# Kernel tuning notes

Measured on AMD Instinct MI355X. Metric: run time of the kernel, lower is better.

## Reference

```python
import jax, jax.numpy as jnp
import numpy as np

B = 4096      # batch
F = 26        # sparse fields
V = 100000    # vocab per field
D = 64        # emb_dim
A = 64        # att_vector
ND = 13       # dense features
FEA = ND + D  # 77, BN / DNN input width
HID = [FEA, 256, 128, 64]
EPS = 1e-5


def setup_inputs() -> dict:
    key = jax.random.key(0)
    ks = jax.random.split(key, 20)
    s = 0.05  # matches .normal_(0, 0.05) init
    inp = {
        "sx": jax.random.randint(ks[0], (B, F), 0, V),
        "dx": jax.random.normal(ks[1], (B, ND), dtype=jnp.float32),
        "emb_table": jax.random.normal(ks[2], (F, V, D), dtype=jnp.float32) * s,
        "att_w_W": jax.random.normal(ks[3], (D, A), dtype=jnp.float32) * s,
        "att_w_b": jnp.zeros((A,), jnp.float32),
        "att_d_W": jax.random.normal(ks[4], (A, 1), dtype=jnp.float32) * s,
        "att_d_b": jnp.zeros((1,), jnp.float32),
        "bn_gamma": jnp.ones((FEA,), jnp.float32),
        "bn_beta": jnp.zeros((FEA,), jnp.float32),
        "w1": jax.random.normal(ks[5], (HID[0], HID[1]), dtype=jnp.float32) * s,
        "b1": jnp.zeros((HID[1],), jnp.float32),
        "w2": jax.random.normal(ks[6], (HID[1], HID[2]), dtype=jnp.float32) * s,
        "b2": jnp.zeros((HID[2],), jnp.float32),
        "w3": jax.random.normal(ks[7], (HID[2], HID[3]), dtype=jnp.float32) * s,
        "b3": jnp.zeros((HID[3],), jnp.float32),
        "wf": jax.random.normal(ks[8], (HID[3], 1), dtype=jnp.float32) * s,
        "bf": jnp.zeros((1,), jnp.float32),
    }
    return inp


def _afm_forward(sx, dx, emb_table, att_w_W, att_w_b, att_d_W, att_d_b,
                 bn_gamma, bn_beta, w1, b1, w2, b2, w3, b3, wf, bf):
    # embedding gather: [B, F, D]
    embeds = emb_table[jnp.arange(F)[None, :], sx]
    # all pairwise field interactions (upper-triangular pairs)
    i1, i2 = np.triu_indices(F, k=1)          # P = F*(F-1)/2 = 325
    bi = embeds[:, i1, :] * embeds[:, i2, :]  # [B, P, D]
    # attention MLP + softmax-weighted sum pooling over pairs
    a = jax.nn.relu(jnp.einsum("bpd,da->bpa", bi, att_w_W) + att_w_b)
    scores = jnp.einsum("bpa,ao->bpo", a, att_d_W) + att_d_b  # [B, P, 1]
    w = jax.nn.softmax(scores, axis=1)
    att_out = jnp.sum(w * bi, axis=1)         # [B, D]
    # concat with dense, batchnorm (training-mode batch stats, biased var)
    x = jnp.concatenate([att_out, dx], axis=-1)  # [B, FEA]
    mu = jnp.mean(x, axis=0)
    var = jnp.mean((x - mu) ** 2, axis=0)
    x = (x - mu) * jax.lax.rsqrt(var + EPS) * bn_gamma + bn_beta
    # DNN tower (dropout=0.0 -> identity) + final linear + sigmoid
    x = jax.nn.relu(x @ w1 + b1)
    x = jax.nn.relu(x @ w2 + b2)
    x = jax.nn.relu(x @ w3 + b3)
    out = jax.nn.sigmoid(x @ wf + bf)
    return jnp.squeeze(out, axis=-1)          # [B]


def reference(sx, dx, emb_table, att_w_W, att_w_b, att_d_W, att_d_b,
              bn_gamma, bn_beta, w1, b1, w2, b2, w3, b3, wf, bf):
    return _afm_forward(sx, dx, emb_table, att_w_W, att_w_b, att_d_W, att_d_b,
                        bn_gamma, bn_beta, w1, b1, w2, b2, w3, b3, wf, bf)
```

## Files before the change

kernel.cpp:

```cpp
#include <hip/hip_runtime.h>
#include <hip/hip_bf16.h>
#include <math.h>

#define BSZ   4096
#define F     26
#define VOC   100000
#define D     64
#define AD    64
#define ND    13
#define FEA   77
#define NPAIR 325
#define NPAD  336
#define MT    21
#define EP    68
#define SCP   384
#define H1    256
#define H2    128
#define H3    64
#define EPSF  1e-5f
#define MROW  8

typedef __attribute__((ext_vector_type(8))) short short8;
typedef __attribute__((ext_vector_type(4))) float f32x4;

union FragU { short8 s; unsigned int u[4]; };

__device__ __forceinline__ unsigned int pk2bf(float a, float b) {
  __hip_bfloat162 h = __float22bfloat162_rn(make_float2(a, b));
  return *reinterpret_cast<unsigned int*>(&h);
}
__device__ __forceinline__ unsigned short f2bf(float f) {
  unsigned int u = __float_as_uint(f);
  u += 0x7fffu + ((u >> 16) & 1u);
  return (unsigned short)(u >> 16);
}
template<int CTRL>
__device__ __forceinline__ float dpp_add(float x) {
  int xi = __builtin_bit_cast(int, x);
  int yi = __builtin_amdgcn_update_dpp(xi, xi, CTRL, 0xf, 0xf, false);
  return x + __builtin_bit_cast(float, yi);
}
__device__ __forceinline__ float row16_sum(float x) {
  x = dpp_add<0xB1>(x);
  x = dpp_add<0x4E>(x);
  x = dpp_add<0x124>(x);
  x = dpp_add<0x128>(x);
  return x;
}

__global__ __launch_bounds__(256, 4) void k_attn(
    const int* __restrict__ sx, const float* __restrict__ dx,
    const float* __restrict__ emb, const float* __restrict__ attW,
    const float* __restrict__ attb, const float* __restrict__ attdW,
    const float* __restrict__ attdb, float* __restrict__ x)
{
  __shared__ __align__(16) float e_all[4][27 * EP];
  __shared__ __align__(16) float sc_all[4][SCP];
  __shared__ unsigned short pt[NPAD];

  const int t    = threadIdx.x;
  const int lane = t & 63;
  const int wv   = t >> 6;
  const int b    = blockIdx.x * 4 + wv;

  for (int p = t; p < NPAD; p += 256) {
    int f1 = 26, f2 = 26;
    if (p < NPAIR) {
      int i = 0, rem = p;
      while (rem >= F - 1 - i) { rem -= F - 1 - i; ++i; }
      f1 = i; f2 = i + 1 + rem;
    }
    pt[p] = (unsigned short)(f1 | (f2 << 8));
  }

  float* e_w  = e_all[wv];
  float* sc_w = sc_all[wv];

  {
    int rowsv[7]; float4 vv[7];
    #pragma unroll
    for (int i = 0; i < 7; ++i) {
      int k = lane + 64 * i, f = k >> 4;
      rowsv[i] = (f < F) ? sx[b * F + f] : 0;
    }
    #pragma unroll
    for (int i = 0; i < 7; ++i) {
      int k = lane + 64 * i, f = k >> 4, q = k & 15;
      float4 v = {0.f, 0.f, 0.f, 0.f};
      if (f < F) v = *(const float4*)&emb[((size_t)f * VOC + rowsv[i]) * D + q * 4];
      vv[i] = v;
    }
    #pragma unroll
    for (int i = 0; i < 7; ++i) {
      int k = lane + 64 * i, f = k >> 4, q = k & 15;
      if (f < 27) *(float4*)&e_w[f * EP + q * 4] = vv[i];
    }
  }

  short8 bfrag[2][4];
  float bj[4], dwj[4];
  {
    const int kb = (lane >> 4) * 8;
    const int cl = lane & 15;
    #pragma unroll
    for (int kk = 0; kk < 2; ++kk)
      #pragma unroll
      for (int n = 0; n < 4; ++n)
        #pragma unroll
        for (int j = 0; j < 8; ++j) {
          int k = kk * 32 + kb + j;
          bfrag[kk][n][j] = (short)f2bf(attW[k * AD + n * 16 + cl]);
        }
    #pragma unroll
    for (int n = 0; n < 4; ++n) {
      bj[n]  = attb[n * 16 + cl];
      dwj[n] = attdW[n * 16 + cl];
    }
  }
  const float db0 = attdb[0];

  __syncthreads();

  const int row16 = lane & 15;
  const int kgrp  = lane >> 4;
  for (int m = 0; m < MT; ++m) {
    const int row = m * 16 + row16;
    const unsigned short pp = pt[row];
    const float* r1 = &e_w[(pp & 0xff) * EP];
    const float* r2 = &e_w[(pp >> 8) * EP];
    FragU a0, a1;
    {
      const int k0 = kgrp * 8;
      float4 x0 = *(const float4*)&r1[k0];
      float4 x1 = *(const float4*)&r1[k0 + 4];
      float4 y0 = *(const float4*)&r2[k0];
      float4 y1 = *(const float4*)&r2[k0 + 4];
      a0.u[0] = pk2bf(x0.x * y0.x, x0.y * y0.y);
      a0.u[1] = pk2bf(x0.z * y0.z, x0.w * y0.w);
      a0.u[2] = pk2bf(x1.x * y1.x, x1.y * y1.y);
      a0.u[3] = pk2bf(x1.z * y1.z, x1.w * y1.w);
      float4 x2 = *(const float4*)&r1[32 + k0];
      float4 x3 = *(const float4*)&r1[32 + k0 + 4];
      float4 y2 = *(const float4*)&r2[32 + k0];
      float4 y3 = *(const float4*)&r2[32 + k0 + 4];
      a1.u[0] = pk2bf(x2.x * y2.x, x2.y * y2.y);
      a1.u[1] = pk2bf(x2.z * y2.z, x2.w * y2.w);
      a1.u[2] = pk2bf(x3.x * y3.x, x3.y * y3.y);
      a1.u[3] = pk2bf(x3.z * y3.z, x3.w * y3.w);
    }
    f32x4 acc[4];
    #pragma unroll
    for (int n = 0; n < 4; ++n) {
      f32x4 z = {0.f, 0.f, 0.f, 0.f};
      acc[n] = __builtin_amdgcn_mfma_f32_16x16x32_bf16(a0.s, bfrag[0][n], z, 0, 0, 0);
      acc[n] = __builtin_amdgcn_mfma_f32_16x16x32_bf16(a1.s, bfrag[1][n], acc[n], 0, 0, 0);
    }
    float v4[4];
    #pragma unroll
    for (int r = 0; r < 4; ++r) {
      float val = 0.f;
      #pragma unroll
      for (int n = 0; n < 4; ++n)
        val += fmaxf(acc[n][r] + bj[n], 0.f) * dwj[n];
      v4[r] = row16_sum(val) + db0;
    }
    if (row16 == 0) {
      float4 o = {v4[0], v4[1], v4[2], v4[3]};
      *(float4*)&sc_w[m * 16 + kgrp * 4] = o;
    }
  }

  float sv[6], ev[6];
  float mx = -1e30f;
  #pragma unroll
  for (int i = 0; i < 6; ++i) {
    int idx = lane + 64 * i;
    sv[i] = (idx < NPAIR) ? sc_w[idx] : -1e30f;
    mx = fmaxf(mx, sv[i]);
  }
  #pragma unroll
  for (int off = 32; off; off >>= 1) mx = fmaxf(mx, __shfl_xor(mx, off));
  float s = 0.f;
  #pragma unroll
  for (int i = 0; i < 6; ++i) {
    int idx = lane + 64 * i;
    ev[i] = (idx < NPAIR) ? __expf(sv[i] - mx) : 0.f;
    s += ev[i];
  }
  #pragma unroll
  for (int off = 32; off; off >>= 1) s += __shfl_xor(s, off);
  const float invZ = 1.f / s;
  #pragma unroll
  for (int i = 0; i < 6; ++i) {
    int idx = lane + 64 * i;
    if (idx < NPAD) sc_w[idx] = ev[i] * invZ;
  }

  const int dblk = lane >> 3;
  const int g    = lane & 7;
  float acc[8] = {0,0,0,0,0,0,0,0};
  for (int it = 0; it < NPAD / 8; ++it) {
    const int p = g + 8 * it;
    const float wgt = sc_w[p];
    const unsigned short pp = pt[p];
    const float* r1 = &e_w[(pp & 0xff) * EP + dblk * 8];
    const float* r2 = &e_w[(pp >> 8) * EP + dblk * 8];
    float4 x0 = *(const float4*)r1;
    float4 x1 = *(const float4*)(r1 + 4);
    float4 y0 = *(const float4*)r2;
    float4 y1 = *(const float4*)(r2 + 4);
    acc[0] = fmaf(wgt, x0.x * y0.x, acc[0]);
    acc[1] = fmaf(wgt, x0.y * y0.y, acc[1]);
    acc[2] = fmaf(wgt, x0.z * y0.z, acc[2]);
    acc[3] = fmaf(wgt, x0.w * y0.w, acc[3]);
    acc[4] = fmaf(wgt, x1.x * y1.x, acc[4]);
    acc[5] = fmaf(wgt, x1.y * y1.y, acc[5]);
    acc[6] = fmaf(wgt, x1.z * y1.z, acc[6]);
    acc[7] = fmaf(wgt, x1.w * y1.w, acc[7]);
  }
  #pragma unroll
  for (int j = 0; j < 8; ++j) {
    acc[j] = dpp_add<0xB1>(acc[j]);
    acc[j] = dpp_add<0x4E>(acc[j]);
    acc[j] = dpp_add<0x124>(acc[j]);
  }
  if (g == 0) {
    float* xo = &x[(size_t)b * FEA + dblk * 8];
    #pragma unroll
    for (int j = 0; j < 8; ++j) xo[j] = acc[j];
  }
  if (lane >= 8 && lane < 8 + ND) {
    x[(size_t)b * FEA + D + (lane - 8)] = dx[b * ND + (lane - 8)];
  }
}

__global__ __launch_bounds__(256) void k_bnstats(
    const float* __restrict__ x, const float* __restrict__ gamma,
    const float* __restrict__ beta, float* __restrict__ scale,
    float* __restrict__ shift)
{
  const int f = blockIdx.x;
  const int t = threadIdx.x;
  const int lane = t & 63;
  const int wv = t >> 6;
  double s = 0.0, s2 = 0.0;
  for (int b = t; b < BSZ; b += 256) {
    float v = x[(size_t)b * FEA + f];
    s += v;
    s2 += (double)v * v;
  }
  #pragma unroll
  for (int off = 32; off; off >>= 1) {
    s += __shfl_xor(s, off);
    s2 += __shfl_xor(s2, off);
  }
  __shared__ double rs[4], rs2[4];
  if (lane == 0) { rs[wv] = s; rs2[wv] = s2; }
  __syncthreads();
  if (t == 0) {
    double S = 0.0, S2 = 0.0;
    #pragma unroll
    for (int i = 0; i < 4; ++i) { S += rs[i]; S2 += rs2[i]; }
    double mu = S / BSZ;
    double var = S2 / BSZ - mu * mu;
    float g = gamma[f];
    float scl = (float)((double)g / sqrt(var + (double)EPSF));
    scale[f] = scl;
    shift[f] = beta[f] - (float)mu * scl;
  }
}

__global__ __launch_bounds__(256) void k_mlp(
    const float* __restrict__ x,
    const float* __restrict__ scale, const float* __restrict__ shift,
    const float* __restrict__ w1, const float* __restrict__ b1,
    const float* __restrict__ w2, const float* __restrict__ b2,
    const float* __restrict__ w3, const float* __restrict__ b3,
    const float* __restrict__ wf, const float* __restrict__ bf,
    float* __restrict__ out)
{
  __shared__ float xn[MROW][80];
  __shared__ float h1s[MROW][H1];
  __shared__ float h2s[MROW][H2];
  __shared__ float h3s[MROW][H3];
  const int t = threadIdx.x;
  const int b0 = blockIdx.x * MROW;

  for (int k = t; k < MROW * FEA; k += 256) {
    int r = k / FEA, f = k % FEA;
    xn[r][f] = x[(size_t)(b0 + r) * FEA + f] * scale[f] + shift[f];
  }
  __syncthreads();

  {
    float acc[MROW];
    const float bb = b1[t];
    #pragma unroll
    for (int r = 0; r < MROW; ++r) acc[r] = bb;
    for (int d = 0; d < FEA; ++d) {
      float wv = w1[d * H1 + t];
      #pragma unroll
      for (int r = 0; r < MROW; ++r) acc[r] = fmaf(xn[r][d], wv, acc[r]);
    }
    #pragma unroll
    for (int r = 0; r < MROW; ++r) h1s[r][t] = fmaxf(acc[r], 0.f);
  }
  __syncthreads();

  {
    const int j = t & 127;
    const int rb = (t >> 7) * 4;
    float acc[4];
    const float bb = b2[j];
    #pragma unroll
    for (int r = 0; r < 4; ++r) acc[r] = bb;
    for (int k = 0; k < H1; ++k) {
      float wv = w2[k * H2 + j];
      #pragma unroll
      for (int r = 0; r < 4; ++r) acc[r] = fmaf(h1s[rb + r][k], wv, acc[r]);
    }
    #pragma unroll
    for (int r = 0; r < 4; ++r) h2s[rb + r][j] = fmaxf(acc[r], 0.f);
  }
  __syncthreads();

  {
    const int j = t & 63;
    const int rb = (t >> 6) * 2;
    float acc[2];
    const float bb = b3[j];
    #pragma unroll
    for (int r = 0; r < 2; ++r) acc[r] = bb;
    for (int k = 0; k < H2; ++k) {
      float wv = w3[k * H3 + j];
      #pragma unroll
      for (int r = 0; r < 2; ++r) acc[r] = fmaf(h2s[rb + r][k], wv, acc[r]);
    }
    #pragma unroll
    for (int r = 0; r < 2; ++r) h3s[rb + r][j] = fmaxf(acc[r], 0.f);
  }
  __syncthreads();

  if (t < MROW) {
    float acc = bf[0];
    for (int k = 0; k < H3; ++k) acc = fmaf(h3s[t][k], wf[k], acc);
    out[b0 + t] = 1.f / (1.f + __expf(-acc));
  }
}

extern "C" void kernel_launch(void* const* d_in, const int* in_sizes, int n_in,
                              void* d_out, int out_size, void* d_ws, size_t ws_size,
                              hipStream_t stream) {
  const int*   sx    = (const int*)  d_in[0];
  const float* dx    = (const float*)d_in[1];
  const float* emb   = (const float*)d_in[2];
  const float* attW  = (const float*)d_in[3];
  const float* attb  = (const float*)d_in[4];
  const float* attdW = (const float*)d_in[5];
  const float* attdb = (const float*)d_in[6];
  const float* gamma = (const float*)d_in[7];
  const float* beta  = (const float*)d_in[8];
  const float* w1    = (const float*)d_in[9];
  const float* b1    = (const float*)d_in[10];
  const float* w2    = (const float*)d_in[11];
  const float* b2    = (const float*)d_in[12];
  const float* w3    = (const float*)d_in[13];
  const float* b3    = (const float*)d_in[14];
  const float* wf    = (const float*)d_in[15];
  const float* bf    = (const float*)d_in[16];
  float* out = (float*)d_out;

  float* x     = (float*)d_ws;
  float* scale = x + (size_t)BSZ * FEA;
  float* shift = scale + FEA;

  k_attn<<<BSZ / 4, 256, 0, stream>>>(sx, dx, emb, attW, attb, attdW, attdb, x);
  k_bnstats<<<FEA, 256, 0, stream>>>(x, gamma, beta, scale, shift);
  k_mlp<<<BSZ / MROW, 256, 0, stream>>>(x, scale, shift, w1, b1, w2, b2, w3, b3,
                                        wf, bf, out);
}
```

Baseline: 72.55 us.

## Fuse attention scoring, online softmax and weighted pooling into one pass

Replaces the three-phase attention (score pairs into shared memory, softmax, then a second pass recomputing pairwise products for the weighted sum) with a single flash-style online-softmax loop. The fp32 pairwise products already built for the MFMA A fragments are reused and accumulated with running-max rescaling, so the shared score buffer and the second LDS sweep over embedding rows go away. In exchange it adds per-tile shuffles for the max and score broadcast, conditional rescaling, and 16 extra accumulator registers per lane, which may raise register pressure under the 4-block launch bound.

```diff
diff --git a/kernel.cpp b/kernel.cpp
--- a/kernel.cpp
+++ b/kernel.cpp
@@ -13,7 +13,6 @@
 #define NPAD  336
 #define MT    21
 #define EP    68
-#define SCP   384
 #define H1    256
 #define H2    128
 #define H3    64
@@ -55,7 +54,6 @@
     const float* __restrict__ attdb, float* __restrict__ x)
 {
   __shared__ __align__(16) float e_all[4][27 * EP];
-  __shared__ __align__(16) float sc_all[4][SCP];
   __shared__ unsigned short pt[NPAD];
 
   const int t    = threadIdx.x;
@@ -73,8 +71,7 @@
     pt[p] = (unsigned short)(f1 | (f2 << 8));
   }
 
-  float* e_w  = e_all[wv];
-  float* sc_w = sc_all[wv];
+  float* e_w = e_all[wv];
 
   {
     int rowsv[7]; float4 vv[7];
@@ -121,33 +118,39 @@
 
   __syncthreads();
 
-  const int row16 = lane & 15;
-  const int kgrp  = lane >> 4;
+  const int row16  = lane & 15;
+  const int kgrp   = lane >> 4;
+  const int kgrp4  = kgrp * 4;
+  const int k0     = kgrp * 8;
+  const int selsrc = ((row16 >> 2) << 4) | row16;
+
+  float pacc_a[8] = {0,0,0,0,0,0,0,0};
+  float pacc_b[8] = {0,0,0,0,0,0,0,0};
+  float m_run = -3.0e38f, l_lane = 0.f;
+
   for (int m = 0; m < MT; ++m) {
-    const int row = m * 16 + row16;
-    const unsigned short pp = pt[row];
+    const int prow = m * 16 + row16;
+    const unsigned short pp = pt[prow];
     const float* r1 = &e_w[(pp & 0xff) * EP];
     const float* r2 = &e_w[(pp >> 8) * EP];
+    float4 x0 = *(const float4*)&r1[k0];
+    float4 x1 = *(const float4*)&r1[k0 + 4];
+    float4 y0 = *(const float4*)&r2[k0];
+    float4 y1 = *(const float4*)&r2[k0 + 4];
+    float4 x2 = *(const float4*)&r1[32 + k0];
+    float4 x3 = *(const float4*)&r1[32 + k0 + 4];
+    float4 y2 = *(const float4*)&r2[32 + k0];
+    float4 y3 = *(const float4*)&r2[32 + k0 + 4];
+    float ba[8] = {x0.x*y0.x, x0.y*y0.y, x0.z*y0.z, x0.w*y0.w,
+                   x1.x*y1.x, x1.y*y1.y, x1.z*y1.z, x1.w*y1.w};
+    float bb[8] = {x2.x*y2.x, x2.y*y2.y, x2.z*y2.z, x2.w*y2.w,
+                   x3.x*y3.x, x3.y*y3.y, x3.z*y3.z, x3.w*y3.w};
     FragU a0, a1;
-    {
-      const int k0 = kgrp * 8;
-      float4 x0 = *(const float4*)&r1[k0];
-      float4 x1 = *(const float4*)&r1[k0 + 4];
-      float4 y0 = *(const float4*)&r2[k0];
-      float4 y1 = *(const float4*)&r2[k0 + 4];
-      a0.u[0] = pk2bf(x0.x * y0.x, x0.y * y0.y);
-      a0.u[1] = pk2bf(x0.z * y0.z, x0.w * y0.w);
-      a0.u[2] = pk2bf(x1.x * y1.x, x1.y * y1.y);
-      a0.u[3] = pk2bf(x1.z * y1.z, x1.w * y1.w);
-      float4 x2 = *(const float4*)&r1[32 + k0];
-      float4 x3 = *(const float4*)&r1[32 + k0 + 4];
-      float4 y2 = *(const float4*)&r2[32 + k0];
-      float4 y3 = *(const float4*)&r2[32 + k0 + 4];
-      a1.u[0] = pk2bf(x2.x * y2.x, x2.y * y2.y);
-      a1.u[1] = pk2bf(x2.z * y2.z, x2.w * y2.w);
-      a1.u[2] = pk2bf(x3.x * y3.x, x3.y * y3.y);
-      a1.u[3] = pk2bf(x3.z * y3.z, x3.w * y3.w);
-    }
+    a0.u[0] = pk2bf(ba[0], ba[1]); a0.u[1] = pk2bf(ba[2], ba[3]);
+    a0.u[2] = pk2bf(ba[4], ba[5]); a0.u[3] = pk2bf(ba[6], ba[7]);
+    a1.u[0] = pk2bf(bb[0], bb[1]); a1.u[1] = pk2bf(bb[2], bb[3]);
+    a1.u[2] = pk2bf(bb[4], bb[5]); a1.u[3] = pk2bf(bb[6], bb[7]);
+
     f32x4 acc[4];
     #pragma unroll
     for (int n = 0; n < 4; ++n) {
@@ -164,70 +167,49 @@
         val += fmaxf(acc[n][r] + bj[n], 0.f) * dwj[n];
       v4[r] = row16_sum(val) + db0;
     }
-    if (row16 == 0) {
-      float4 o = {v4[0], v4[1], v4[2], v4[3]};
-      *(float4*)&sc_w[m * 16 + kgrp * 4] = o;
-    }
-  }
-
-  float sv[6], ev[6];
-  float mx = -1e30f;
-  #pragma unroll
-  for (int i = 0; i < 6; ++i) {
-    int idx = lane + 64 * i;
-    sv[i] = (idx < NPAIR) ? sc_w[idx] : -1e30f;
-    mx = fmaxf(mx, sv[i]);
-  }
-  #pragma unroll
-  for (int off = 32; off; off >>= 1) mx = fmaxf(mx, __shfl_xor(mx, off));
-  float s = 0.f;
-  #pragma unroll
-  for (int i = 0; i < 6; ++i) {
-    int idx = lane + 64 * i;
-    ev[i] = (idx < NPAIR) ? __expf(sv[i] - mx) : 0.f;
-    s += ev[i];
-  }
-  #pragma unroll
-  for (int off = 32; off; off >>= 1) s += __shfl_xor(s, off);
-  const float invZ = 1.f / s;
-  #pragma unroll
-  for (int i = 0; i < 6; ++i) {
-    int idx = lane + 64 * i;
-    if (idx < NPAD) sc_w[idx] = ev[i] * invZ;
-  }
-
-  const int dblk = lane >> 3;
-  const int g    = lane & 7;
-  float acc[8] = {0,0,0,0,0,0,0,0};
-  for (int it = 0; it < NPAD / 8; ++it) {
-    const int p = g + 8 * it;
-    const float wgt = sc_w[p];
-    const unsigned short pp = pt[p];
-    const float* r1 = &e_w[(pp & 0xff) * EP + dblk * 8];
-    const float* r2 = &e_w[(pp >> 8) * EP + dblk * 8];
-    float4 x0 = *(const float4*)r1;
-    float4 x1 = *(const float4*)(r1 + 4);
-    float4 y0 = *(const float4*)r2;
-    float4 y1 = *(const float4*)(r2 + 4);
-    acc[0] = fmaf(wgt, x0.x * y0.x, acc[0]);
-    acc[1] = fmaf(wgt, x0.y * y0.y, acc[1]);
-    acc[2] = fmaf(wgt, x0.z * y0.z, acc[2]);
-    acc[3] = fmaf(wgt, x0.w * y0.w, acc[3]);
-    acc[4] = fmaf(wgt, x1.x * y1.x, acc[4]);
-    acc[5] = fmaf(wgt, x1.y * y1.y, acc[5]);
-    acc[6] = fmaf(wgt, x1.z * y1.z, acc[6]);
-    acc[7] = fmaf(wgt, x1.w * y1.w, acc[7]);
-  }
+    float sel = v4[0];
+    sel = ((row16 & 3) == 1) ? v4[1] : sel;
+    sel = ((row16 & 3) == 2) ? v4[2] : sel;
+    sel = ((row16 & 3) == 3) ? v4[3] : sel;
+    const float s_p = __shfl(sel, selsrc);
+    float lm = -3.0e38f;
+    #pragma unroll
+    for (int r = 0; r < 4; ++r) {
+      int p = m * 16 + kgrp4 + r;
+      if (p < NPAIR) lm = fmaxf(lm, v4[r]);
+    }
+    lm = fmaxf(lm, __shfl_xor(lm, 16));
+    lm = fmaxf(lm, __shfl_xor(lm, 32));
+    if (lm > m_run) {
+      const float scl = __expf(m_run - lm);
+      l_lane *= scl;
+      #pragma unroll
+      for (int j = 0; j < 8; ++j) { pacc_a[j] *= scl; pacc_b[j] *= scl; }
+      m_run = lm;
+    }
+    const float w = (prow < NPAIR) ? __expf(s_p - m_run) : 0.f;
+    l_lane += w;
+    #pragma unroll
+    for (int j = 0; j < 8; ++j) {
+      pacc_a[j] = fmaf(w, ba[j], pacc_a[j]);
+      pacc_b[j] = fmaf(w, bb[j], pacc_b[j]);
+    }
+  }
+
+  const float l_tot = row16_sum(l_lane);
+  const float invZ = 1.f / l_tot;
   #pragma unroll
   for (int j = 0; j < 8; ++j) {
-    acc[j] = dpp_add<0xB1>(acc[j]);
-    acc[j] = dpp_add<0x4E>(acc[j]);
-    acc[j] = dpp_add<0x124>(acc[j]);
-  }
-  if (g == 0) {
-    float* xo = &x[(size_t)b * FEA + dblk * 8];
-    #pragma unroll
-    for (int j = 0; j < 8; ++j) xo[j] = acc[j];
+    pacc_a[j] = row16_sum(pacc_a[j]);
+    pacc_b[j] = row16_sum(pacc_b[j]);
+  }
+  if (row16 == 0) {
+    float* xo = &x[(size_t)b * FEA + kgrp * 8];
+    #pragma unroll
+    for (int j = 0; j < 8; ++j) xo[j] = pacc_a[j] * invZ;
+    float* xo2 = &x[(size_t)b * FEA + 32 + kgrp * 8];
+    #pragma unroll
+    for (int j = 0; j < 8; ++j) xo2[j] = pacc_b[j] * invZ;
   }
   if (lane >= 8 && lane < 8 + ND) {
     x[(size_t)b * FEA + D + (lane - 8)] = dx[b * ND + (lane - 8)];
```

Result: slower. 74.46 us (+2.6%).

## Store gathered embeddings as bf16 in LDS and halve MLP rows per block

Applied to the files above, without the earlier changes.

The attention kernel now packs gathered embedding rows into bf16 in shared memory with a smaller row stride, so LDS traffic for pair products and pooling is halved and occupancy may rise. Products are formed from the bf16-unpacked values, which loses precision in the weighted-sum pooling that was previously fp32. Separately, the MLP kernel processes 4 rows per block instead of 8, doubling grid size for more parallelism, and adds unroll pragmas.

```diff
diff --git a/kernel.cpp b/kernel.cpp
--- a/kernel.cpp
+++ b/kernel.cpp
@@ -12,13 +12,12 @@
 #define NPAIR 325
 #define NPAD  336
 #define MT    21
-#define EP    68
-#define SCP   384
+#define ERS   36
 #define H1    256
 #define H2    128
 #define H3    64
 #define EPSF  1e-5f
-#define MROW  8
+#define MROW  4
 
 typedef __attribute__((ext_vector_type(8))) short short8;
 typedef __attribute__((ext_vector_type(4))) float f32x4;
@@ -33,6 +32,12 @@
   unsigned int u = __float_as_uint(f);
   u += 0x7fffu + ((u >> 16) & 1u);
   return (unsigned short)(u >> 16);
+}
+__device__ __forceinline__ float bflo(unsigned int u) {
+  return __uint_as_float(u << 16);
+}
+__device__ __forceinline__ float bfhi(unsigned int u) {
+  return __uint_as_float(u & 0xffff0000u);
 }
 template<int CTRL>
 __device__ __forceinline__ float dpp_add(float x) {
@@ -54,8 +59,8 @@
     const float* __restrict__ attb, const float* __restrict__ attdW,
     const float* __restrict__ attdb, float* __restrict__ x)
 {
-  __shared__ __align__(16) float e_all[4][27 * EP];
-  __shared__ __align__(16) float sc_all[4][SCP];
+  __shared__ __align__(16) unsigned int e_all[4][27 * ERS];
+  __shared__ __align__(16) float sc_all[4][NPAD];
   __shared__ unsigned short pt[NPAD];
 
   const int t    = threadIdx.x;
@@ -73,7 +78,7 @@
     pt[p] = (unsigned short)(f1 | (f2 << 8));
   }
 
-  float* e_w  = e_all[wv];
+  unsigned int* e_w = e_all[wv];
   float* sc_w = sc_all[wv];
 
   {
@@ -93,7 +98,10 @@
     #pragma unroll
     for (int i = 0; i < 7; ++i) {
       int k = lane + 64 * i, f = k >> 4, q = k & 15;
-      if (f < 27) *(float4*)&e_w[f * EP + q * 4] = vv[i];
+      if (f < 27) {
+        uint2 o = { pk2bf(vv[i].x, vv[i].y), pk2bf(vv[i].z, vv[i].w) };
+        *(uint2*)&e_w[f * ERS + 2 * q] = o;
+      }
     }
   }
 
@@ -123,31 +131,26 @@
 
   const int row16 = lane & 15;
   const int kgrp  = lane >> 4;
+  const int ku    = kgrp * 4;
   for (int m = 0; m < MT; ++m) {
-    const int row = m * 16 + row16;
-    const unsigned short pp = pt[row];
-    const float* r1 = &e_w[(pp & 0xff) * EP];
-    const float* r2 = &e_w[(pp >> 8) * EP];
+    const int prow = m * 16 + row16;
+    const unsigned short pp = pt[prow];
+    const unsigned int* r1 = &e_w[(pp & 0xff) * ERS];
+    const unsigned int* r2 = &e_w[(pp >> 8) * ERS];
+    uint4 u1a = *(const uint4*)&r1[ku];
+    uint4 u2a = *(const uint4*)&r2[ku];
+    uint4 u1b = *(const uint4*)&r1[16 + ku];
+    uint4 u2b = *(const uint4*)&r2[16 + ku];
     FragU a0, a1;
-    {
-      const int k0 = kgrp * 8;
-      float4 x0 = *(const float4*)&r1[k0];
-      float4 x1 = *(const float4*)&r1[k0 + 4];
-      float4 y0 = *(const float4*)&r2[k0];
-      float4 y1 = *(const float4*)&r2[k0 + 4];
-      a0.u[0] = pk2bf(x0.x * y0.x, x0.y * y0.y);
-      a0.u[1] = pk2bf(x0.z * y0.z, x0.w * y0.w);
-      a0.u[2] = pk2bf(x1.x * y1.x, x1.y * y1.y);
-      a0.u[3] = pk2bf(x1.z * y1.z, x1.w * y1.w);
-      float4 x2 = *(const float4*)&r1[32 + k0];
-      float4 x3 = *(const float4*)&r1[32 + k0 + 4];
-      float4 y2 = *(const float4*)&r2[32 + k0];
-      float4 y3 = *(const float4*)&r2[32 + k0 + 4];
-      a1.u[0] = pk2bf(x2.x * y2.x, x2.y * y2.y);
-      a1.u[1] = pk2bf(x2.z * y2.z, x2.w * y2.w);
-      a1.u[2] = pk2bf(x3.x * y3.x, x3.y * y3.y);
-      a1.u[3] = pk2bf(x3.z * y3.z, x3.w * y3.w);
-    }
+    a0.u[0] = pk2bf(bflo(u1a.x)*bflo(u2a.x), bfhi(u1a.x)*bfhi(u2a.x));
+    a0.u[1] = pk2bf(bflo(u1a.y)*bflo(u2a.y), bfhi(u1a.y)*bfhi(u2a.y));
+    a0.u[2] = pk2bf(bflo(u1a.z)*bflo(u2a.z), bfhi(u1a.z)*bfhi(u2a.z));
+    a0.u[3] = pk2bf(bflo(u1a.w)*bflo(u2a.w), bfhi(u1a.w)*bfhi(u2a.w));
+    a1.u[0] = pk2bf(bflo(u1b.x)*bflo(u2b.x), bfhi(u1b.x)*bfhi(u2b.x));
+    a1.u[1] = pk2bf(bflo(u1b.y)*bflo(u2b.y), bfhi(u1b.y)*bfhi(u2b.y));
+    a1.u[2] = pk2bf(bflo(u1b.z)*bflo(u2b.z), bfhi(u1b.z)*bfhi(u2b.z));
+    a1.u[3] = pk2bf(bflo(u1b.w)*bflo(u2b.w), bfhi(u1b.w)*bfhi(u2b.w));
+
     f32x4 acc[4];
     #pragma unroll
     for (int n = 0; n < 4; ++n) {
@@ -203,20 +206,16 @@
     const int p = g + 8 * it;
     const float wgt = sc_w[p];
     const unsigned short pp = pt[p];
-    const float* r1 = &e_w[(pp & 0xff) * EP + dblk * 8];
-    const float* r2 = &e_w[(pp >> 8) * EP + dblk * 8];
-    float4 x0 = *(const float4*)r1;
-    float4 x1 = *(const float4*)(r1 + 4);
-    float4 y0 = *(const float4*)r2;
-    float4 y1 = *(const float4*)(r2 + 4);
-    acc[0] = fmaf(wgt, x0.x * y0.x, acc[0]);
-    acc[1] = fmaf(wgt, x0.y * y0.y, acc[1]);
-    acc[2] = fmaf(wgt, x0.z * y0.z, acc[2]);
-    acc[3] = fmaf(wgt, x0.w * y0.w, acc[3]);
-    acc[4] = fmaf(wgt, x1.x * y1.x, acc[4]);
-    acc[5] = fmaf(wgt, x1.y * y1.y, acc[5]);
-    acc[6] = fmaf(wgt, x1.z * y1.z, acc[6]);
-    acc[7] = fmaf(wgt, x1.w * y1.w, acc[7]);
+    uint4 w1v = *(const uint4*)&e_w[(pp & 0xff) * ERS + dblk * 4];
+    uint4 w2v = *(const uint4*)&e_w[(pp >> 8) * ERS + dblk * 4];
+    acc[0] = fmaf(wgt, bflo(w1v.x) * bflo(w2v.x), acc[0]);
+    acc[1] = fmaf(wgt, bfhi(w1v.x) * bfhi(w2v.x), acc[1]);
+    acc[2] = fmaf(wgt, bflo(w1v.y) * bflo(w2v.y), acc[2]);
+    acc[3] = fmaf(wgt, bfhi(w1v.y) * bfhi(w2v.y), acc[3]);
+    acc[4] = fmaf(wgt, bflo(w1v.z) * bflo(w2v.z), acc[4]);
+    acc[5] = fmaf(wgt, bfhi(w1v.z) * bfhi(w2v.z), acc[5]);
+    acc[6] = fmaf(wgt, bflo(w1v.w) * bflo(w2v.w), acc[6]);
+    acc[7] = fmaf(wgt, bfhi(w1v.w) * bfhi(w2v.w), acc[7]);
   }
   #pragma unroll
   for (int j = 0; j < 8; ++j) {
@@ -297,6 +296,7 @@
     const float bb = b1[t];
     #pragma unroll
     for (int r = 0; r < MROW; ++r) acc[r] = bb;
+    #pragma unroll 8
     for (int d = 0; d < FEA; ++d) {
       float wv = w1[d * H1 + t];
       #pragma unroll
@@ -309,40 +309,35 @@
 
   {
     const int j = t & 127;
-    const int rb = (t >> 7) * 4;
-    float acc[4];
+    const int rb = (t >> 7) * 2;
+    float acc[2];
     const float bb = b2[j];
-    #pragma unroll
-    for (int r = 0; r < 4; ++r) acc[r] = bb;
+    acc[0] = bb; acc[1] = bb;
+    #pragma unroll 8
     for (int k = 0; k < H1; ++k) {
       float wv = w2[k * H2 + j];
-      #pragma unroll
-      for (int r = 0; r < 4; ++r) acc[r] = fmaf(h1s[rb + r][k], wv, acc[r]);
-    }
-    #pragma unroll
-    for (int r = 0; r < 4; ++r) h2s[rb + r][j] = fmaxf(acc[r], 0.f);
+      acc[0] = fmaf(h1s[rb + 0][k], wv, acc[0]);
+      acc[1] = fmaf(h1s[rb + 1][k], wv, acc[1]);
+    }
+    h2s[rb + 0][j] = fmaxf(acc[0], 0.f);
+    h2s[rb + 1][j] = fmaxf(acc[1], 0.f);
   }
   __syncthreads();
 
   {
     const int j = t & 63;
-    const int rb = (t >> 6) * 2;
-    float acc[2];
-    const float bb = b3[j];
-    #pragma unroll
-    for (int r = 0; r < 2; ++r) acc[r] = bb;
-    for (int k = 0; k < H2; ++k) {
-      float wv = w3[k * H3 + j];
-      #pragma unroll
-      for (int r = 0; r < 2; ++r) acc[r] = fmaf(h2s[rb + r][k], wv, acc[r]);
-    }
-    #pragma unroll
-    for (int r = 0; r < 2; ++r) h3s[rb + r][j] = fmaxf(acc[r], 0.f);
+    const int r = t >> 6;
+    float acc = b3[j];
+    #pragma unroll 8
+    for (int k = 0; k < H2; ++k)
+      acc = fmaf(h2s[r][k], w3[k * H3 + j], acc);
+    h3s[r][j] = fmaxf(acc, 0.f);
   }
   __syncthreads();
 
   if (t < MROW) {
     float acc = bf[0];
+    #pragma unroll 8
     for (int k = 0; k < H3; ++k) acc = fmaf(h3s[t][k], wf[k], acc);
     out[b0 + t] = 1.f / (1.f + __expf(-acc));
   }
```

Measured after the change: 79.87 us. 1.1x slower.

## Fuse BN statistics into attention kernel and pool pairs in registers

Applied to the files above, without the earlier changes.

Removes the separate BN-stats kernel. The attention kernel now accumulates per-feature sum and sum-of-squares through atomics into 8 bucketed partial arrays, and the MLP kernel finalizes the scale and shift itself. Each lane keeps its embedding column in registers, so the weighted pair pooling becomes a fully unrolled 325-step loop using readlane broadcasts of the softmax weights instead of shared-memory loads. This saves a launch and a pass over x, at the cost of a memset, atomic contention, fp32 (rather than double) variance with the E[x^2]-mu^2 form, and much higher register pressure from the unrolled loop.

```diff
diff --git a/kernel.cpp b/kernel.cpp
--- a/kernel.cpp
+++ b/kernel.cpp
@@ -13,7 +13,6 @@
 #define NPAD  336
 #define MT    21
 #define EP    68
-#define SCP   384
 #define H1    256
 #define H2    128
 #define H3    64
@@ -47,21 +46,27 @@
   x = dpp_add<0x128>(x);
   return x;
 }
+__device__ __forceinline__ float bcast_lane(float v, int l) {
+  return __builtin_bit_cast(float,
+      __builtin_amdgcn_readlane(__builtin_bit_cast(int, v), l));
+}
 
 __global__ __launch_bounds__(256, 4) void k_attn(
     const int* __restrict__ sx, const float* __restrict__ dx,
     const float* __restrict__ emb, const float* __restrict__ attW,
     const float* __restrict__ attb, const float* __restrict__ attdW,
-    const float* __restrict__ attdb, float* __restrict__ x)
+    const float* __restrict__ attdb, float* __restrict__ x,
+    float* __restrict__ partS, float* __restrict__ partQ)
 {
   __shared__ __align__(16) float e_all[4][27 * EP];
-  __shared__ __align__(16) float sc_all[4][SCP];
+  __shared__ __align__(16) float sc_all[4][NPAD];
+  __shared__ float xblk[4][80];
   __shared__ unsigned short pt[NPAD];
 
   const int t    = threadIdx.x;
   const int lane = t & 63;
   const int wv   = t >> 6;
-  const int b    = blockIdx.x * 4 + wv;
+  const int b    = __builtin_amdgcn_readfirstlane(blockIdx.x * 4 + wv);
 
   for (int p = t; p < NPAD; p += 256) {
     int f1 = 26, f2 = 26;
@@ -76,25 +81,18 @@
   float* e_w  = e_all[wv];
   float* sc_w = sc_all[wv];
 
-  {
-    int rowsv[7]; float4 vv[7];
-    #pragma unroll
-    for (int i = 0; i < 7; ++i) {
-      int k = lane + 64 * i, f = k >> 4;
-      rowsv[i] = (f < F) ? sx[b * F + f] : 0;
-    }
-    #pragma unroll
-    for (int i = 0; i < 7; ++i) {
-      int k = lane + 64 * i, f = k >> 4, q = k & 15;
-      float4 v = {0.f, 0.f, 0.f, 0.f};
-      if (f < F) v = *(const float4*)&emb[((size_t)f * VOC + rowsv[i]) * D + q * 4];
-      vv[i] = v;
-    }
-    #pragma unroll
-    for (int i = 0; i < 7; ++i) {
-      int k = lane + 64 * i, f = k >> 4, q = k & 15;
-      if (f < 27) *(float4*)&e_w[f * EP + q * 4] = vv[i];
-    }
+  float ef[F];
+  {
+    const int* sxb = sx + b * F;
+    int rows[F];
+    #pragma unroll
+    for (int f = 0; f < F; ++f) rows[f] = sxb[f];
+    #pragma unroll
+    for (int f = 0; f < F; ++f)
+      ef[f] = emb[((size_t)f * VOC + rows[f]) * D + lane];
+    #pragma unroll
+    for (int f = 0; f < F; ++f) e_w[f * EP + lane] = ef[f];
+    e_w[26 * EP + lane] = 0.f;
   }
 
   short8 bfrag[2][4];
@@ -123,31 +121,30 @@
 
   const int row16 = lane & 15;
   const int kgrp  = lane >> 4;
+  const int k0    = kgrp * 8;
   for (int m = 0; m < MT; ++m) {
-    const int row = m * 16 + row16;
-    const unsigned short pp = pt[row];
+    const int prow = m * 16 + row16;
+    const unsigned short pp = pt[prow];
     const float* r1 = &e_w[(pp & 0xff) * EP];
     const float* r2 = &e_w[(pp >> 8) * EP];
+    float4 x0 = *(const float4*)&r1[k0];
+    float4 x1 = *(const float4*)&r1[k0 + 4];
+    float4 y0 = *(const float4*)&r2[k0];
+    float4 y1 = *(const float4*)&r2[k0 + 4];
+    float4 x2 = *(const float4*)&r1[32 + k0];
+    float4 x3 = *(const float4*)&r1[32 + k0 + 4];
+    float4 y2 = *(const float4*)&r2[32 + k0];
+    float4 y3 = *(const float4*)&r2[32 + k0 + 4];
     FragU a0, a1;
-    {
-      const int k0 = kgrp * 8;
-      float4 x0 = *(const float4*)&r1[k0];
-      float4 x1 = *(const float4*)&r1[k0 + 4];
-      float4 y0 = *(const float4*)&r2[k0];
-      float4 y1 = *(const float4*)&r2[k0 + 4];
-      a0.u[0] = pk2bf(x0.x * y0.x, x0.y * y0.y);
-      a0.u[1] = pk2bf(x0.z * y0.z, x0.w * y0.w);
-      a0.u[2] = pk2bf(x1.x * y1.x, x1.y * y1.y);
-      a0.u[3] = pk2bf(x1.z * y1.z, x1.w * y1.w);
-      float4 x2 = *(const float4*)&r1[32 + k0];
-      float4 x3 = *(const float4*)&r1[32 + k0 + 4];
-      float4 y2 = *(const float4*)&r2[32 + k0];
-      float4 y3 = *(const float4*)&r2[32 + k0 + 4];
-      a1.u[0] = pk2bf(x2.x * y2.x, x2.y * y2.y);
-      a1.u[1] = pk2bf(x2.z * y2.z, x2.w * y2.w);
-      a1.u[2] = pk2bf(x3.x * y3.x, x3.y * y3.y);
-      a1.u[3] = pk2bf(x3.z * y3.z, x3.w * y3.w);
-    }
+    a0.u[0] = pk2bf(x0.x*y0.x, x0.y*y0.y);
+    a0.u[1] = pk2bf(x0.z*y0.z, x0.w*y0.w);
+    a0.u[2] = pk2bf(x1.x*y1.x, x1.y*y1.y);
+    a0.u[3] = pk2bf(x1.z*y1.z, x1.w*y1.w);
+    a1.u[0] = pk2bf(x2.x*y2.x, x2.y*y2.y);
+    a1.u[1] = pk2bf(x2.z*y2.z, x2.w*y2.w);
+    a1.u[2] = pk2bf(x3.x*y3.x, x3.y*y3.y);
+    a1.u[3] = pk2bf(x3.z*y3.z, x3.w*y3.w);
+
     f32x4 acc[4];
     #pragma unroll
     for (int n = 0; n < 4; ++n) {
@@ -190,95 +187,56 @@
   #pragma unroll
   for (int off = 32; off; off >>= 1) s += __shfl_xor(s, off);
   const float invZ = 1.f / s;
-  #pragma unroll
-  for (int i = 0; i < 6; ++i) {
-    int idx = lane + 64 * i;
-    if (idx < NPAD) sc_w[idx] = ev[i] * invZ;
-  }
-
-  const int dblk = lane >> 3;
-  const int g    = lane & 7;
-  float acc[8] = {0,0,0,0,0,0,0,0};
-  for (int it = 0; it < NPAD / 8; ++it) {
-    const int p = g + 8 * it;
-    const float wgt = sc_w[p];
-    const unsigned short pp = pt[p];
-    const float* r1 = &e_w[(pp & 0xff) * EP + dblk * 8];
-    const float* r2 = &e_w[(pp >> 8) * EP + dblk * 8];
-    float4 x0 = *(const float4*)r1;
-    float4 x1 = *(const float4*)(r1 + 4);
-    float4 y0 = *(const float4*)r2;
-    float4 y1 = *(const float4*)(r2 + 4);
-    acc[0] = fmaf(wgt, x0.x * y0.x, acc[0]);
-    acc[1] = fmaf(wgt, x0.y * y0.y, acc[1]);
-    acc[2] = fmaf(wgt, x0.z * y0.z, acc[2]);
-    acc[3] = fmaf(wgt, x0.w * y0.w, acc[3]);
-    acc[4] = fmaf(wgt, x1.x * y1.x, acc[4]);
-    acc[5] = fmaf(wgt, x1.y * y1.y, acc[5]);
-    acc[6] = fmaf(wgt, x1.z * y1.z, acc[6]);
-    acc[7] = fmaf(wgt, x1.w * y1.w, acc[7]);
-  }
-  #pragma unroll
-  for (int j = 0; j < 8; ++j) {
-    acc[j] = dpp_add<0xB1>(acc[j]);
-    acc[j] = dpp_add<0x4E>(acc[j]);
-    acc[j] = dpp_add<0x124>(acc[j]);
-  }
-  if (g == 0) {
-    float* xo = &x[(size_t)b * FEA + dblk * 8];
-    #pragma unroll
-    for (int j = 0; j < 8; ++j) xo[j] = acc[j];
-  }
-  if (lane >= 8 && lane < 8 + ND) {
-    x[(size_t)b * FEA + D + (lane - 8)] = dx[b * ND + (lane - 8)];
-  }
-}
-
-__global__ __launch_bounds__(256) void k_bnstats(
-    const float* __restrict__ x, const float* __restrict__ gamma,
-    const float* __restrict__ beta, float* __restrict__ scale,
-    float* __restrict__ shift)
-{
-  const int f = blockIdx.x;
-  const int t = threadIdx.x;
-  const int lane = t & 63;
-  const int wv = t >> 6;
-  double s = 0.0, s2 = 0.0;
-  for (int b = t; b < BSZ; b += 256) {
-    float v = x[(size_t)b * FEA + f];
-    s += v;
-    s2 += (double)v * v;
-  }
-  #pragma unroll
-  for (int off = 32; off; off >>= 1) {
-    s += __shfl_xor(s, off);
-    s2 += __shfl_xor(s2, off);
-  }
-  __shared__ double rs[4], rs2[4];
-  if (lane == 0) { rs[wv] = s; rs2[wv] = s2; }
-  __syncthreads();
-  if (t == 0) {
-    double S = 0.0, S2 = 0.0;
-    #pragma unroll
-    for (int i = 0; i < 4; ++i) { S += rs[i]; S2 += rs2[i]; }
-    double mu = S / BSZ;
-    double var = S2 / BSZ - mu * mu;
-    float g = gamma[f];
-    float scl = (float)((double)g / sqrt(var + (double)EPSF));
-    scale[f] = scl;
-    shift[f] = beta[f] - (float)mu * scl;
+
+  float pa0 = 0.f, pa1 = 0.f, pa2 = 0.f, pa3 = 0.f;
+  {
+    int p = 0;
+    #pragma unroll
+    for (int f1 = 0; f1 < F - 1; ++f1) {
+      #pragma unroll
+      for (int f2 = f1 + 1; f2 < F; ++f2) {
+        const float w = bcast_lane(ev[p >> 6], p & 63);
+        const float prod = ef[f1] * ef[f2];
+        if ((p & 3) == 0)      pa0 = fmaf(w, prod, pa0);
+        else if ((p & 3) == 1) pa1 = fmaf(w, prod, pa1);
+        else if ((p & 3) == 2) pa2 = fmaf(w, prod, pa2);
+        else                   pa3 = fmaf(w, prod, pa3);
+        ++p;
+      }
+    }
+  }
+  const float att = ((pa0 + pa1) + (pa2 + pa3)) * invZ;
+
+  x[(size_t)b * FEA + lane] = att;
+  xblk[wv][lane] = att;
+  if (lane < ND) {
+    float dv = dx[b * ND + lane];
+    x[(size_t)b * FEA + D + lane] = dv;
+    xblk[wv][D + lane] = dv;
+  }
+  __syncthreads();
+
+  if (t < FEA) {
+    float x0 = xblk[0][t], x1 = xblk[1][t], x2 = xblk[2][t], x3 = xblk[3][t];
+    float sS = (x0 + x1) + (x2 + x3);
+    float sQ = (x0 * x0 + x1 * x1) + (x2 * x2 + x3 * x3);
+    const int bkt = (blockIdx.x & 7) * 80 + t;
+    atomicAdd(&partS[bkt], sS);
+    atomicAdd(&partQ[bkt], sQ);
   }
 }
 
 __global__ __launch_bounds__(256) void k_mlp(
     const float* __restrict__ x,
-    const float* __restrict__ scale, const float* __restrict__ shift,
+    const float* __restrict__ partS, const float* __restrict__ partQ,
+    const float* __restrict__ gamma, const float* __restrict__ beta,
     const float* __restrict__ w1, const float* __restrict__ b1,
     const float* __restrict__ w2, const float* __restrict__ b2,
     const float* __restrict__ w3, const float* __restrict__ b3,
     const float* __restrict__ wf, const float* __restrict__ bf,
     float* __restrict__ out)
 {
+  __shared__ float scs[80], shs[80];
   __shared__ float xn[MROW][80];
   __shared__ float h1s[MROW][H1];
   __shared__ float h2s[MROW][H2];
@@ -286,9 +244,24 @@
   const int t = threadIdx.x;
   const int b0 = blockIdx.x * MROW;
 
+  if (t < FEA) {
+    float S = 0.f, Q = 0.f;
+    #pragma unroll
+    for (int k = 0; k < 8; ++k) {
+      S += partS[k * 80 + t];
+      Q += partQ[k * 80 + t];
+    }
+    float mu  = S * (1.f / BSZ);
+    float var = Q * (1.f / BSZ) - mu * mu;
+    float scl = gamma[t] * rsqrtf(var + EPSF);
+    scs[t] = scl;
+    shs[t] = beta[t] - mu * scl;
+  }
+  __syncthreads();
+
   for (int k = t; k < MROW * FEA; k += 256) {
     int r = k / FEA, f = k % FEA;
-    xn[r][f] = x[(size_t)(b0 + r) * FEA + f] * scale[f] + shift[f];
+    xn[r][f] = x[(size_t)(b0 + r) * FEA + f] * scs[f] + shs[f];
   }
   __syncthreads();
 
@@ -329,15 +302,14 @@
     const int rb = (t >> 6) * 2;
     float acc[2];
     const float bb = b3[j];
-    #pragma unroll
-    for (int r = 0; r < 2; ++r) acc[r] = bb;
+    acc[0] = bb; acc[1] = bb;
     for (int k = 0; k < H2; ++k) {
       float wv = w3[k * H3 + j];
-      #pragma unroll
-      for (int r = 0; r < 2; ++r) acc[r] = fmaf(h2s[rb + r][k], wv, acc[r]);
-    }
-    #pragma unroll
-    for (int r = 0; r < 2; ++r) h3s[rb + r][j] = fmaxf(acc[r], 0.f);
+      acc[0] = fmaf(h2s[rb + 0][k], wv, acc[0]);
+      acc[1] = fmaf(h2s[rb + 1][k], wv, acc[1]);
+    }
+    h3s[rb + 0][j] = fmaxf(acc[0], 0.f);
+    h3s[rb + 1][j] = fmaxf(acc[1], 0.f);
   }
   __syncthreads();
 
@@ -371,11 +343,12 @@
   float* out = (float*)d_out;
 
   float* x     = (float*)d_ws;
-  float* scale = x + (size_t)BSZ * FEA;
-  float* shift = scale + FEA;
-
-  k_attn<<<BSZ / 4, 256, 0, stream>>>(sx, dx, emb, attW, attb, attdW, attdb, x);
-  k_bnstats<<<FEA, 256, 0, stream>>>(x, gamma, beta, scale, shift);
-  k_mlp<<<BSZ / MROW, 256, 0, stream>>>(x, scale, shift, w1, b1, w2, b2, w3, b3,
-                                        wf, bf, out);
-}
+  float* partS = x + (size_t)BSZ * FEA;
+  float* partQ = partS + 8 * 80;
+
+  hipMemsetAsync(partS, 0, 2 * 8 * 80 * sizeof(float), stream);
+  k_attn<<<BSZ / 4, 256, 0, stream>>>(sx, dx, emb, attW, attb, attdW, attdb,
+                                      x, partS, partQ);
+  k_mlp<<<BSZ / MROW, 256, 0, stream>>>(x, partS, partQ, gamma, beta,
+                                        w1, b1, w2, b2, w3, b3, wf, bf, out);
+}
```

Result: faster. 68.21 us (-6.0%).
